# Optimization experiments

Hardware: AMD Instinct MI355X
Metric: run time of the kernel (lower is better)

The kernel has to match this reference:

```python
import jax, jax.numpy as jnp
import numpy as np

B, S, D, H = 32, 64, 256, 8
HD = D // H
NS = S + 1
TH = 0.5
LN_EPS = 1e-5


def _lin(k, out_d, in_d, gain=1.0):
    lim = gain * np.sqrt(6.0 / (in_d + out_d))
    return jax.random.uniform(k, (out_d, in_d), minval=-lim, maxval=lim, dtype=jnp.float32)


def setup_inputs() -> dict:
    key = jax.random.key(0)
    ks = jax.random.split(key, 16)
    g = 1.0 / np.sqrt(2.0)
    return {
        'desc_embeddings': jax.random.normal(ks[0], (B, S, D), dtype=jnp.float32),
        'name_value_embeddings': jax.random.normal(ks[1], (B, NS, D), dtype=jnp.float32),
        'Wg': _lin(ks[2], D, D), 'bg': jnp.zeros((D,), jnp.float32),
        'Wq': _lin(ks[3], D, D, g), 'bq': jnp.zeros((D,), jnp.float32),
        'Wk': _lin(ks[4], D, D, g), 'bk': jnp.zeros((D,), jnp.float32),
        'Wv': _lin(ks[5], D, D, g), 'bv': jnp.zeros((D,), jnp.float32),
        'We1': _lin(ks[6], D, 2 * D), 'be1': jnp.zeros((D,), jnp.float32),
        'lng': jnp.ones((D,), jnp.float32), 'lnb': jnp.zeros((D,), jnp.float32),
        'We2': _lin(ks[7], D, D), 'be2': jnp.zeros((D,), jnp.float32),
        'Wa': _lin(ks[8], 1, 3 * HD, g), 'ba': jnp.zeros((1,), jnp.float32),
        'Wo': _lin(ks[9], D, D, g), 'bo': jnp.zeros((D,), jnp.float32),
        'tb': jnp.zeros((1,), jnp.float32),
    }


def reference(desc_embeddings, name_value_embeddings, Wg, bg, Wq, bq, Wk, bk, Wv, bv,
              We1, be1, lng, lnb, We2, be2, Wa, ba, Wo, bo, tb):
    # 1. Global topology
    desc = desc_embeddings @ Wg.T + bg                      # [B,S,D]
    dn = desc / jnp.linalg.norm(desc, axis=-1, keepdims=True)
    gsim = jnp.einsum('bid,bjd->bij', dn, dn)
    gt = jax.nn.sigmoid(gsim + tb[0])
    # straight-through threshold
    A = (gt > TH).astype(gt.dtype) - jax.lax.stop_gradient(gt) + gt
    # 2. Sample-wise similarity
    var = name_value_embeddings[:, 1:, :]
    vn = var / jnp.linalg.norm(var, axis=-1, keepdims=True)
    ssim = jnp.einsum('bid,bjd->bij', vn, vn)
    A = A * (1.0 - jnp.eye(S, dtype=A.dtype))               # no self-interaction
    adjacency = jax.nn.softmax(A * ssim, axis=-1)
    # 4. Edge attrs & adjacency (scatter-assembled, CLS at index 0)
    var_edge = jnp.concatenate([
        jnp.broadcast_to(desc[:, :, None, :], (B, S, S, D)),
        jnp.broadcast_to(desc[:, None, :, :], (B, S, S, D))], axis=-1)  # [B,S,S,2D]
    cls_edge = jnp.concatenate([desc, desc], axis=-1)       # [B,S,2D]
    ea = jnp.zeros((B, NS, NS, 2 * D), jnp.float32)
    ea = ea.at[:, 1:, 1:].set(var_edge).at[:, 0, 1:].set(cls_edge).at[:, 1:, 0].set(cls_edge)
    na = jnp.zeros((B, NS, NS), jnp.float32)
    na = na.at[:, 1:, 1:].set(adjacency).at[:, 0, 1:].set(1.0)
    # 5. Attention
    q = (name_value_embeddings @ Wq.T + bq).reshape(B, NS, H, HD).transpose(0, 2, 1, 3)
    k = (name_value_embeddings @ Wk.T + bk).reshape(B, NS, H, HD).transpose(0, 2, 1, 3)
    v = (name_value_embeddings @ Wv.T + bv).reshape(B, NS, H, HD).transpose(0, 2, 1, 3)
    h = ea @ We1.T + be1
    mu = h.mean(axis=-1, keepdims=True)
    sig = ((h - mu) ** 2).mean(axis=-1, keepdims=True)
    h = (h - mu) / jnp.sqrt(sig + LN_EPS) * lng + lnb
    e = jax.nn.relu(h) @ We2.T + be2                        # [B,NS,NS,D]
    e = e.reshape(B, NS, NS, H, HD).transpose(0, 3, 1, 2, 4)  # [B,H,NS,NS,HD]
    e = e * na[:, None, :, :, None]
    # attn_proj(concat(q_i, k_j, e_ij)) decomposed into three dot products
    wq, wk_, we = Wa[0, :HD], Wa[0, HD:2 * HD], Wa[0, 2 * HD:]
    sq = jnp.einsum('bhid,d->bhi', q, wq)
    sk = jnp.einsum('bhjd,d->bhj', k, wk_)
    se = jnp.einsum('bhijd,d->bhij', e, we)
    scores = sq[:, :, :, None] + sk[:, :, None, :] + se + ba[0]
    scores = scores + (na[:, None, :, :] == 0).astype(scores.dtype) * -1e9
    aw = jax.nn.softmax(scores, axis=-1)                    # [B,H,NS,NS]
    ctx = jnp.einsum('bhij,bhjd->bhid', aw, v).transpose(0, 2, 1, 3).reshape(B, NS, D)
    out = ctx @ Wo.T + bo
    return (out, aw)
```

## Files before the change

### kernel.cpp

```cpp
#include <hip/hip_runtime.h>
#include <hip/hip_bf16.h>

#define BB 32
#define SS 64
#define DD 256
#define HH 8
#define HDIM 32
#define NSS 65
#define LN_EPS 1e-5f

#define OFF_DESC   0u
#define OFF_DESCT  524288u
#define OFF_U      1048576u
#define OFF_VT     1572864u
#define OFF_VART   2097152u
#define OFF_VBUF   2621440u
#define OFF_SQ     3153920u
#define OFF_SK     3170560u
#define OFF_CTX    3187200u
#define OFF_WGT    3719680u
#define OFF_WE1AT  3785216u
#define OFF_WE1BT  3850752u
#define OFF_WVT    3916288u
#define OFF_WOT    3981824u
#define OFF_CUT    4047360u
#define OFF_CVT    4112896u
#define OFF_BU     4178432u
#define OFF_BV     4178688u
#define OFF_WQF    4178944u
#define OFF_WKF    4180992u
#define OFF_CVEC   4183040u
#define OFF_RND    4183072u
#define OFF_RNV    4185120u
#define OFF_PKG    4187168u
#define OFF_PKM    4187680u

template <int R>
__device__ __forceinline__ void gemmR_body(const float* __restrict__ in,
                                           const float* __restrict__ WT,
                                           const float* __restrict__ bias,
                                           float* __restrict__ out,
                                           float* __restrict__ outT,
                                           int r0, int addBias, float* vals) {
    int o = threadIdx.x;
    const float* __restrict__ x = in + (size_t)r0 * DD;
    float acc[R];
    #pragma unroll
    for (int r = 0; r < R; ++r) acc[r] = 0.f;
    #pragma unroll 4
    for (int k = 0; k < DD; ++k) {
        float w = WT[(size_t)k * DD + o];
        #pragma unroll
        for (int r = 0; r < R; ++r)
            acc[r] = fmaf(x[r * DD + k], w, acc[r]);
    }
    float bb = addBias ? bias[o] : 0.f;
    #pragma unroll
    for (int r = 0; r < R; ++r) vals[r] = acc[r] + bb;
    if (out) {
        #pragma unroll
        for (int r = 0; r < R; ++r)
            out[(size_t)(r0 + r) * DD + o] = vals[r];
    }
    if (outT) {
        size_t base = (size_t)(r0 >> 6) * 16384 + (size_t)(o >> 2) * 256 + (o & 3);
        int j0 = r0 & 63;
        #pragma unroll
        for (int r = 0; r < R; ++r)
            outT[base + (size_t)(j0 + r) * 4] = vals[r];
    }
}

__global__ __launch_bounds__(256) void prep_a(
    const float* __restrict__ Wg, const float* __restrict__ We1,
    const float* __restrict__ Wv, const float* __restrict__ Wo,
    const float* __restrict__ Wq, const float* __restrict__ bq,
    const float* __restrict__ Wk, const float* __restrict__ bk,
    const float* __restrict__ We2, const float* __restrict__ be2,
    const float* __restrict__ Wa, const float* __restrict__ lng,
    const float* __restrict__ lnb,
    float* __restrict__ WgT, float* __restrict__ We1aT, float* __restrict__ We1bT,
    float* __restrict__ WvT, float* __restrict__ WoT,
    float* __restrict__ wqf, float* __restrict__ wkf,
    float* __restrict__ PKg, float* __restrict__ PKm, float* __restrict__ cvec) {
    __shared__ float t[64][65];
    int blk = blockIdx.x;
    if (blk < 80) {
        int which = blk >> 4, t16 = blk & 15;
        const float* src; float* dst; int ld, c0;
        if (which == 0)      { src = Wg;  dst = WgT;   ld = 256; c0 = 0; }
        else if (which == 1) { src = We1; dst = We1aT; ld = 512; c0 = 0; }
        else if (which == 2) { src = We1; dst = We1bT; ld = 512; c0 = 256; }
        else if (which == 3) { src = Wv;  dst = WvT;   ld = 256; c0 = 0; }
        else                 { src = Wo;  dst = WoT;   ld = 256; c0 = 0; }
        int to = t16 & 3, tk = t16 >> 2;
        int tx = threadIdx.x & 63, ty = threadIdx.x >> 6;
        #pragma unroll
        for (int r = ty; r < 64; r += 4)
            t[r][tx] = src[(size_t)(to * 64 + r) * ld + c0 + tk * 64 + tx];
        __syncthreads();
        #pragma unroll
        for (int r = ty; r < 64; r += 4)
            dst[(size_t)(tk * 64 + r) * DD + to * 64 + tx] = t[tx][r];
    } else if (blk < 88) {
        int h = blk - 80, in = threadIdx.x;
        float aq = 0.f, ak = 0.f, ae = 0.f;
        #pragma unroll
        for (int d = 0; d < HDIM; ++d) {
            aq = fmaf(Wq[(h * HDIM + d) * DD + in], Wa[d], aq);
            ak = fmaf(Wk[(h * HDIM + d) * DD + in], Wa[HDIM + d], ak);
            ae = fmaf(We2[(h * HDIM + d) * DD + in], Wa[2 * HDIM + d], ae);
        }
        wqf[h * DD + in] = aq;
        wkf[h * DD + in] = ak;
        PKm[in * HH + h] = ae;
        if (in == 0) {
            float cq = 0.f, ck = 0.f, ce = 0.f;
            for (int d = 0; d < HDIM; ++d) {
                cq = fmaf(bq[h * HDIM + d], Wa[d], cq);
                ck = fmaf(bk[h * HDIM + d], Wa[HDIM + d], ck);
                ce = fmaf(be2[h * HDIM + d], Wa[2 * HDIM + d], ce);
            }
            cvec[h] = cq; cvec[8 + h] = ck; cvec[16 + h] = ce;
        }
    } else {
        int d = threadIdx.x;
        PKg[d * 2] = lng[d];
        PKg[d * 2 + 1] = lnb[d];
    }
}

__global__ __launch_bounds__(256) void prep_b(
    const float* __restrict__ WgT, const float* __restrict__ We1aT,
    const float* __restrict__ We1bT, const float* __restrict__ bg,
    const float* __restrict__ be1,
    float* __restrict__ CuT, float* __restrict__ CvT,
    float* __restrict__ bu, float* __restrict__ bv) {
    float vals[16];
    int blk = blockIdx.x;
    if (blk < 16) gemmR_body<16>(WgT, We1aT, nullptr, CuT, nullptr, blk * 16, 0, vals);
    else if (blk < 32) gemmR_body<16>(WgT, We1bT, nullptr, CvT, nullptr, (blk - 16) * 16, 0, vals);
    else if (blk == 32) {
        int o = threadIdx.x;
        float a = be1[o];
        for (int m = 0; m < DD; ++m) a = fmaf(We1aT[(size_t)m * DD + o], bg[m], a);
        bu[o] = a;
    } else {
        int o = threadIdx.x;
        float a = 0.f;
        for (int m = 0; m < DD; ++m) a = fmaf(We1bT[(size_t)m * DD + o], bg[m], a);
        bv[o] = a;
    }
}

__global__ __launch_bounds__(256) void proj_kernel(
    const float* __restrict__ X, const float* __restrict__ nve,
    const float* __restrict__ WgT, const float* __restrict__ CuT,
    const float* __restrict__ CvT, const float* __restrict__ WvT,
    const float* __restrict__ bg, const float* __restrict__ bu,
    const float* __restrict__ bv, const float* __restrict__ bwv,
    const float* __restrict__ wqf, const float* __restrict__ wkf,
    const float* __restrict__ cvec,
    float* __restrict__ desc, float* __restrict__ descT,
    float* __restrict__ U, float* __restrict__ VT,
    float* __restrict__ varT, float* __restrict__ vbuf,
    float* __restrict__ sq, float* __restrict__ sk,
    float* __restrict__ rnd, float* __restrict__ rnv) {
    __shared__ float red[4][8];
    float vals[8];
    int blk = blockIdx.x;
    if (blk < 256) {
        gemmR_body<8>(X, WgT, bg, desc, descT, blk * 8, 1, vals);
        int w = threadIdx.x >> 6, lane = threadIdx.x & 63;
        #pragma unroll
        for (int r = 0; r < 8; ++r) {
            float s2 = vals[r] * vals[r];
            #pragma unroll
            for (int off = 32; off; off >>= 1) s2 += __shfl_xor(s2, off);
            if (lane == 0) red[w][r] = s2;
        }
        __syncthreads();
        if (threadIdx.x < 8) {
            float s = red[0][threadIdx.x] + red[1][threadIdx.x] +
                      red[2][threadIdx.x] + red[3][threadIdx.x];
            rnd[blk * 8 + threadIdx.x] = 1.f / sqrtf(s);
        }
    } else if (blk < 512) {
        gemmR_body<8>(X, CuT, bu, U, nullptr, (blk - 256) * 8, 1, vals);
    } else if (blk < 768) {
        gemmR_body<8>(X, CvT, bv, nullptr, VT, (blk - 512) * 8, 1, vals);
    } else if (blk < 1028) {
        gemmR_body<8>(nve, WvT, bwv, vbuf, nullptr, (blk - 768) * 8, 1, vals);
    } else if (blk < 1158) {
        int r0 = (blk - 1028) * 16;
        int lr = threadIdx.x >> 4, tq = threadIdx.x & 15;
        int g = r0 + lr, b = g / NSS, ii = g % NSS;
        const float* __restrict__ x = nve + (size_t)g * DD;
        const float* __restrict__ wv = ((tq < 8) ? wqf : wkf) + (tq & 7) * DD;
        float acc = 0.f;
        #pragma unroll 8
        for (int k = 0; k < DD; ++k) acc = fmaf(x[k], wv[k], acc);
        int h = tq & 7;
        if (tq < 8) sq[(size_t)(b * HH + h) * NSS + ii] = acc + cvec[h];
        else        sk[(size_t)(b * HH + h) * NSS + ii] = acc + cvec[8 + h];
    } else if (blk < 1286) {
        int r0 = (blk - 1158) * 16;
        int lr = threadIdx.x >> 4, tq = threadIdx.x & 15;
        int g = r0 + lr, b = g >> 6, s = g & 63;
        const float* __restrict__ x = nve + (size_t)(b * NSS + 1 + s) * DD;
        float ssum = 0.f;
        for (int k = tq; k < DD; k += 16) ssum = fmaf(x[k], x[k], ssum);
        ssum += __shfl_xor(ssum, 1);
        ssum += __shfl_xor(ssum, 2);
        ssum += __shfl_xor(ssum, 4);
        ssum += __shfl_xor(ssum, 8);
        if (tq == 0) rnv[g] = 1.f / sqrtf(ssum);
    } else {
        int b = blk - 1286;
        int d = threadIdx.x;
        size_t base = (size_t)b * 16384 + (size_t)(d >> 2) * 256 + (d & 3);
        const float* __restrict__ src = nve + ((size_t)b * NSS + 1) * DD + d;
        #pragma unroll 4
        for (int j = 0; j < 64; ++j)
            varT[base + (size_t)j * 4] = src[(size_t)j * DD];
    }
}

__global__ __launch_bounds__(256) void se_attn_kernel(
    const float* __restrict__ desc, const float* __restrict__ descT,
    const float* __restrict__ nve,  const float* __restrict__ varT,
    const float* __restrict__ U,    const float* __restrict__ VT,
    const float* __restrict__ vbuf,
    const float* __restrict__ rnd,  const float* __restrict__ rnv,
    const float* __restrict__ sq,   const float* __restrict__ sk,
    const float* __restrict__ PKg,  const float* __restrict__ PKm,
    const float* __restrict__ cvec, const float* __restrict__ ba,
    const float* __restrict__ tb,
    float* __restrict__ aw, float* __restrict__ ctx) {
    __shared__ float SH[4224];
    int t = blockIdx.x >> 5, b = blockIdx.x & 31;
    int w = threadIdx.x >> 6, lane = threadIdx.x & 63;
    float bav = ba[0];

    if (t < 16) {
        int iu = __builtin_amdgcn_readfirstlane(t * 4 + w);
        int i = iu + 1;
        const float4* __restrict__ dT4  = (const float4*)(descT + (size_t)b * 16384);
        const float4* __restrict__ vrT4 = (const float4*)(varT  + (size_t)b * 16384);
        const float4* __restrict__ vt4  = (const float4*)(VT    + (size_t)b * 16384);
        const float4* __restrict__ di4 = (const float4*)(desc + (size_t)(b * SS + iu) * DD);
        const float4* __restrict__ vi4 = (const float4*)(nve + (size_t)(b * NSS + 1 + iu) * DD);
        const float4* __restrict__ ui4 = (const float4*)(U + (size_t)(b * SS + iu) * DD);

        float gd = 0.f, vd = 0.f, ssum = 0.f, s2 = 0.f;
        #pragma unroll 4
        for (int f = 0; f < 64; ++f) {
            float4 a = dT4[f * 64 + lane];  float4 u1 = di4[f];
            float4 c = vrT4[f * 64 + lane]; float4 u2 = vi4[f];
            float4 v = vt4[f * 64 + lane];  float4 u = ui4[f];
            gd = fmaf(a.x, u1.x, gd); gd = fmaf(a.y, u1.y, gd);
            gd = fmaf(a.z, u1.z, gd); gd = fmaf(a.w, u1.w, gd);
            vd = fmaf(c.x, u2.x, vd); vd = fmaf(c.y, u2.y, vd);
            vd = fmaf(c.z, u2.z, vd); vd = fmaf(c.w, u2.w, vd);
            float t0 = v.x + u.x, t1 = v.y + u.y, t2 = v.z + u.z, t3 = v.w + u.w;
            ssum += (t0 + t1) + (t2 + t3);
            s2 = fmaf(t0, t0, s2); s2 = fmaf(t1, t1, s2);
            s2 = fmaf(t2, t2, s2); s2 = fmaf(t3, t3, s2);
        }
        float gsim = gd * rnd[b * SS + iu] * rnd[b * SS + lane];
        float ssim = vd * rnv[b * SS + iu] * rnv[b * SS + lane];
        bool flag = (gsim + tb[0] > 0.f) && (iu != lane);
        float P = flag ? ssim : 0.f;
        float e = __expf(P);
        float s = e;
        #pragma unroll
        for (int off = 32; off; off >>= 1) s += __shfl_xor(s, off);
        float nav = e / s;
        float mu = ssum * (1.f / DD);
        float var = fmaf(-mu, mu, s2 * (1.f / DD));
        float rstd = rsqrtf(var + LN_EPS);

        float p[HH];
        #pragma unroll
        for (int h = 0; h < HH; ++h) p[h] = 0.f;
        #pragma unroll 2
        for (int f = 0; f < 64; ++f) {
            float4 v = vt4[f * 64 + lane]; float4 u = ui4[f];
            const float4* __restrict__ pg = (const float4*)(PKg + 8 * f);
            float4 pg0 = pg[0], pg1 = pg[1];
            float tv[4] = {v.x + u.x, v.y + u.y, v.z + u.z, v.w + u.w};
            float gv[4] = {pg0.x, pg0.z, pg1.x, pg1.z};
            float bv_[4] = {pg0.y, pg0.w, pg1.y, pg1.w};
            #pragma unroll
            for (int c = 0; c < 4; ++c) {
                const float4* __restrict__ m4 = (const float4*)(PKm + (size_t)(4 * f + c) * HH);
                float4 mlo = m4[0], mhi = m4[1];
                float xn = fmaf((tv[c] - mu) * rstd, gv[c], bv_[c]);
                float r = fmaxf(xn, 0.f);
                p[0] = fmaf(r, mlo.x, p[0]); p[1] = fmaf(r, mlo.y, p[1]);
                p[2] = fmaf(r, mlo.z, p[2]); p[3] = fmaf(r, mlo.w, p[3]);
                p[4] = fmaf(r, mhi.x, p[4]); p[5] = fmaf(r, mhi.y, p[5]);
                p[6] = fmaf(r, mhi.z, p[6]); p[7] = fmaf(r, mhi.w, p[7]);
            }
        }

        float* awL = SH + w * 528;
        #pragma unroll
        for (int h = 0; h < HH; ++h) {
            float sev = nav * (p[h] + cvec[16 + h]);
            float sc = sq[(size_t)(b * HH + h) * NSS + i] +
                       sk[(size_t)(b * HH + h) * NSS + 1 + lane] + sev + bav;
            float m = sc;
            #pragma unroll
            for (int off = 32; off; off >>= 1) m = fmaxf(m, __shfl_xor(m, off));
            float e2 = __expf(sc - m);
            float tot = e2;
            #pragma unroll
            for (int off = 32; off; off >>= 1) tot += __shfl_xor(tot, off);
            float aval = e2 / tot;
            float* awrow = aw + ((size_t)(b * HH + h) * NSS + i) * NSS;
            awrow[1 + lane] = aval;
            if (lane == 0) awrow[0] = 0.f;
            awL[h * 66 + lane] = aval;
        }
        const float* __restrict__ awh = awL + (lane >> 3) * 66;
        const float4* __restrict__ vb4 = (const float4*)(vbuf + ((size_t)b * NSS + 1) * DD);
        float cx = 0.f, cy = 0.f, cz = 0.f, cw = 0.f;
        #pragma unroll 4
        for (int j = 0; j < 64; ++j) {
            float a = awh[j];
            float4 v = vb4[(size_t)j * 64 + lane];
            cx = fmaf(a, v.x, cx); cy = fmaf(a, v.y, cy);
            cz = fmaf(a, v.z, cz); cw = fmaf(a, v.w, cw);
        }
        *(float4*)(ctx + ((size_t)(b * NSS) + i) * DD + 4 * lane) =
            make_float4(cx, cy, cz, cw);
    } else {
        float* tile = SH;
        int dloc = lane & 31, jh = lane >> 5;
        float ss = 0.f, s2 = 0.f;
        for (int c = 0; c < 4; ++c) {
            for (int jr = w; jr < 64; jr += 4)
                tile[jr * 65 + lane] = U[(size_t)(b * SS + jr) * DD + c * 64 + lane];
            __syncthreads();
            #pragma unroll 8
            for (int dd = 0; dd < 64; ++dd) {
                int d = c * 64 + dd;
                float u = tile[lane * 65 + dd];
                float v = VT[(size_t)b * 16384 + (size_t)(d >> 2) * 256 + lane * 4 + (d & 3)];
                float t2 = u + v; ss += t2; s2 = fmaf(t2, t2, s2);
            }
            __syncthreads();
        }
        float mu = ss * (1.f / DD);
        float va = fmaf(-mu, mu, s2 * (1.f / DD));
        float rstd = rsqrtf(va + LN_EPS);
        float p[HH];
        #pragma unroll
        for (int h = 0; h < HH; ++h) p[h] = 0.f;
        for (int c = 0; c < 4; ++c) {
            for (int jr = w; jr < 64; jr += 4)
                tile[jr * 65 + lane] = U[(size_t)(b * SS + jr) * DD + c * 64 + lane];
            __syncthreads();
            #pragma unroll 4
            for (int dd = 0; dd < 64; ++dd) {
                int d = c * 64 + dd;
                float u = tile[lane * 65 + dd];
                float v = VT[(size_t)b * 16384 + (size_t)(d >> 2) * 256 + lane * 4 + (d & 3)];
                float t2 = u + v;
                float rv = fmaxf(fmaf((t2 - mu) * rstd, PKg[d * 2], PKg[d * 2 + 1]), 0.f);
                const float* __restrict__ m8 = PKm + (size_t)d * HH;
                #pragma unroll
                for (int h = 0; h < HH; ++h) p[h] = fmaf(rv, m8[h], p[h]);
            }
            __syncthreads();
        }
        float sel0 = 0.f, sel1 = 0.f;
        #pragma unroll
        for (int h = 0; h < HH; ++h) {
            if (h == w * 2)     sel0 = p[h];
            if (h == w * 2 + 1) sel1 = p[h];
        }
        #pragma unroll
        for (int q = 0; q < 2; ++q) {
            int h = w * 2 + q;
            float dot = q ? sel1 : sel0;
            float sev = dot + cvec[16 + h];
            float skh = sk[(size_t)(b * HH + h) * NSS + 1 + lane];
            float sc = sq[(size_t)(b * HH + h) * NSS] + skh + sev + bav;
            float m = sc;
            #pragma unroll
            for (int off = 32; off; off >>= 1) m = fmaxf(m, __shfl_xor(m, off));
            float e = __expf(sc - m), s = e;
            #pragma unroll
            for (int off = 32; off; off >>= 1) s += __shfl_xor(s, off);
            float aval = e / s;
            float* awrow = aw + ((size_t)(b * HH + h) * NSS) * NSS;
            awrow[1 + lane] = aval;
            if (lane == 0) awrow[0] = 0.f;
            float acc = 0.f;
            #pragma unroll
            for (int j2 = 0; j2 < 32; ++j2) {
                int jj = j2 * 2 + jh;
                float a = __shfl(aval, jj);
                acc = fmaf(a, vbuf[((size_t)(b * NSS) + 1 + jj) * DD + h * HDIM + dloc], acc);
            }
            acc += __shfl_xor(acc, 32);
            if (lane < 32)
                ctx[(size_t)(b * NSS) * DD + h * HDIM + dloc] = acc;
        }
    }
}

__global__ __launch_bounds__(256) void outgemm_kernel(
    const float* __restrict__ ctx, const float* __restrict__ WoT,
    const float* __restrict__ bo, float* __restrict__ out) {
    float vals[8];
    gemmR_body<8>(ctx, WoT, bo, out, nullptr, blockIdx.x * 8, 1, vals);
}

extern "C" void kernel_launch(void* const* d_in, const int* in_sizes, int n_in,
                              void* d_out, int out_size, void* d_ws, size_t ws_size,
                              hipStream_t stream) {
    const float* desc_emb = (const float*)d_in[0];
    const float* nve      = (const float*)d_in[1];
    const float* Wg  = (const float*)d_in[2];
    const float* bg  = (const float*)d_in[3];
    const float* Wq  = (const float*)d_in[4];
    const float* bq  = (const float*)d_in[5];
    const float* Wk  = (const float*)d_in[6];
    const float* bk  = (const float*)d_in[7];
    const float* Wv  = (const float*)d_in[8];
    const float* bv_in = (const float*)d_in[9];
    const float* We1 = (const float*)d_in[10];
    const float* be1 = (const float*)d_in[11];
    const float* lng = (const float*)d_in[12];
    const float* lnb = (const float*)d_in[13];
    const float* We2 = (const float*)d_in[14];
    const float* be2 = (const float*)d_in[15];
    const float* Wa  = (const float*)d_in[16];
    const float* ba  = (const float*)d_in[17];
    const float* Wo  = (const float*)d_in[18];
    const float* bo  = (const float*)d_in[19];
    const float* tb  = (const float*)d_in[20];

    float* ws    = (float*)d_ws;
    float* desc  = ws + OFF_DESC;
    float* descT = ws + OFF_DESCT;
    float* U     = ws + OFF_U;
    float* VT    = ws + OFF_VT;
    float* varT  = ws + OFF_VART;
    float* vbuf  = ws + OFF_VBUF;
    float* sq    = ws + OFF_SQ;
    float* sk    = ws + OFF_SK;
    float* ctx   = ws + OFF_CTX;
    float* WgT   = ws + OFF_WGT;
    float* We1aT = ws + OFF_WE1AT;
    float* We1bT = ws + OFF_WE1BT;
    float* WvT   = ws + OFF_WVT;
    float* WoT   = ws + OFF_WOT;
    float* CuT   = ws + OFF_CUT;
    float* CvT   = ws + OFF_CVT;
    float* bu    = ws + OFF_BU;
    float* bv    = ws + OFF_BV;
    float* wqf   = ws + OFF_WQF;
    float* wkf   = ws + OFF_WKF;
    float* cvec  = ws + OFF_CVEC;
    float* rnd   = ws + OFF_RND;
    float* rnv   = ws + OFF_RNV;
    float* PKg   = ws + OFF_PKG;
    float* PKm   = ws + OFF_PKM;

    float* out = (float*)d_out;
    float* aw  = out + (size_t)BB * NSS * DD;

    prep_a<<<89, 256, 0, stream>>>(Wg, We1, Wv, Wo, Wq, bq, Wk, bk, We2, be2,
                                   Wa, lng, lnb,
                                   WgT, We1aT, We1bT, WvT, WoT,
                                   wqf, wkf, PKg, PKm, cvec);
    prep_b<<<34, 256, 0, stream>>>(WgT, We1aT, We1bT, bg, be1, CuT, CvT, bu, bv);
    proj_kernel<<<1318, 256, 0, stream>>>(desc_emb, nve, WgT, CuT, CvT, WvT,
                                          bg, bu, bv, bv_in, wqf, wkf, cvec,
                                          desc, descT, U, VT, varT, vbuf,
                                          sq, sk, rnd, rnv);
    se_attn_kernel<<<544, 256, 0, stream>>>(desc, descT, nve, varT, U, VT,
                                            vbuf, rnd, rnv, sq, sk,
                                            PKg, PKm, cvec, ba, tb, aw, ctx);
    outgemm_kernel<<<260, 256, 0, stream>>>(ctx, WoT, bo, out);
}
```

Before: 146.2 us.

## Split adjacency/LayerNorm stats into separate kernel and halve heads per wave

Moves the per-row adjacency softmax and LayerNorm mean/rstd computation into a new adjln_kernel that writes them to scratch buffers that reuse dead weight-transpose workspace. The edge-score kernel then assigns each wave half of the heads (4 instead of 8), using a repacked interleaved gamma/beta/head-weight table, and splits the context reduction across two half-waves joined with a shuffle. This doubles the number of blocks to raise parallelism and cut per-thread register pressure. The cost is an extra launch, extra global round trips, and the LN/U+V reads being repeated for each head half.

```diff
diff --git a/kernel.cpp b/kernel.cpp
--- a/kernel.cpp
+++ b/kernel.cpp
@@ -34,6 +34,7 @@
 #define OFF_RNV    4185120u
 #define OFF_PKG    4187168u
 #define OFF_PKM    4187680u
+#define OFF_PKH    4189728u
 
 template <int R>
 __device__ __forceinline__ void gemmR_body(const float* __restrict__ in,
@@ -82,7 +83,8 @@
     float* __restrict__ WgT, float* __restrict__ We1aT, float* __restrict__ We1bT,
     float* __restrict__ WvT, float* __restrict__ WoT,
     float* __restrict__ wqf, float* __restrict__ wkf,
-    float* __restrict__ PKg, float* __restrict__ PKm, float* __restrict__ cvec) {
+    float* __restrict__ PKg, float* __restrict__ PKm, float* __restrict__ PKH,
+    float* __restrict__ cvec) {
     __shared__ float t[64][65];
     int blk = blockIdx.x;
     if (blk < 80) {
@@ -114,6 +116,7 @@
         wqf[h * DD + in] = aq;
         wkf[h * DD + in] = ak;
         PKm[in * HH + h] = ae;
+        PKH[((size_t)(h >> 2) * 256 + in) * 8 + 2 + (h & 3)] = ae;
         if (in == 0) {
             float cq = 0.f, ck = 0.f, ce = 0.f;
             for (int d = 0; d < HDIM; ++d) {
@@ -127,6 +130,14 @@
         int d = threadIdx.x;
         PKg[d * 2] = lng[d];
         PKg[d * 2 + 1] = lnb[d];
+        #pragma unroll
+        for (int hq = 0; hq < 2; ++hq) {
+            size_t base = ((size_t)hq * 256 + d) * 8;
+            PKH[base + 0] = lng[d];
+            PKH[base + 1] = lnb[d];
+            PKH[base + 6] = 0.f;
+            PKH[base + 7] = 0.f;
+        }
     }
 }
 
@@ -226,88 +237,106 @@
     }
 }
 
-__global__ __launch_bounds__(256) void se_attn_kernel(
+__global__ __launch_bounds__(256) void adjln_kernel(
     const float* __restrict__ desc, const float* __restrict__ descT,
     const float* __restrict__ nve,  const float* __restrict__ varT,
     const float* __restrict__ U,    const float* __restrict__ VT,
+    const float* __restrict__ rnd,  const float* __restrict__ rnv,
+    const float* __restrict__ tb,
+    float* __restrict__ navbuf, float* __restrict__ mubuf,
+    float* __restrict__ rstdbuf) {
+    int t = blockIdx.x >> 5, b = blockIdx.x & 31;
+    int w = threadIdx.x >> 6, lane = threadIdx.x & 63;
+    int iu = __builtin_amdgcn_readfirstlane(t * 4 + w);
+    const float4* __restrict__ dT4  = (const float4*)(descT + (size_t)b * 16384);
+    const float4* __restrict__ vrT4 = (const float4*)(varT  + (size_t)b * 16384);
+    const float4* __restrict__ vt4  = (const float4*)(VT    + (size_t)b * 16384);
+    const float4* __restrict__ di4 = (const float4*)(desc + (size_t)(b * SS + iu) * DD);
+    const float4* __restrict__ vi4 = (const float4*)(nve + (size_t)(b * NSS + 1 + iu) * DD);
+    const float4* __restrict__ ui4 = (const float4*)(U + (size_t)(b * SS + iu) * DD);
+    float gd = 0.f, vd = 0.f, ssum = 0.f, s2 = 0.f;
+    #pragma unroll 4
+    for (int f = 0; f < 64; ++f) {
+        float4 a = dT4[f * 64 + lane];  float4 u1 = di4[f];
+        float4 c = vrT4[f * 64 + lane]; float4 u2 = vi4[f];
+        float4 v = vt4[f * 64 + lane];  float4 u = ui4[f];
+        gd = fmaf(a.x, u1.x, gd); gd = fmaf(a.y, u1.y, gd);
+        gd = fmaf(a.z, u1.z, gd); gd = fmaf(a.w, u1.w, gd);
+        vd = fmaf(c.x, u2.x, vd); vd = fmaf(c.y, u2.y, vd);
+        vd = fmaf(c.z, u2.z, vd); vd = fmaf(c.w, u2.w, vd);
+        float t0 = v.x + u.x, t1 = v.y + u.y, t2 = v.z + u.z, t3 = v.w + u.w;
+        ssum += (t0 + t1) + (t2 + t3);
+        s2 = fmaf(t0, t0, s2); s2 = fmaf(t1, t1, s2);
+        s2 = fmaf(t2, t2, s2); s2 = fmaf(t3, t3, s2);
+    }
+    float gsim = gd * rnd[b * SS + iu] * rnd[b * SS + lane];
+    float ssim = vd * rnv[b * SS + iu] * rnv[b * SS + lane];
+    bool flag = (gsim + tb[0] > 0.f) && (iu != lane);
+    float P = flag ? ssim : 0.f;
+    float e = __expf(P);
+    float s = e;
+    #pragma unroll
+    for (int off = 32; off; off >>= 1) s += __shfl_xor(s, off);
+    float nav = e / s;
+    float mu = ssum * (1.f / DD);
+    float var = fmaf(-mu, mu, s2 * (1.f / DD));
+    float rstd = rsqrtf(var + LN_EPS);
+    size_t rowoff = (size_t)(b * SS + iu) * 64 + lane;
+    navbuf[rowoff] = nav;
+    mubuf[rowoff] = mu;
+    rstdbuf[rowoff] = rstd;
+}
+
+__global__ __launch_bounds__(256) void se_attn_kernel(
+    const float* __restrict__ U,    const float* __restrict__ VT,
     const float* __restrict__ vbuf,
-    const float* __restrict__ rnd,  const float* __restrict__ rnv,
     const float* __restrict__ sq,   const float* __restrict__ sk,
+    const float* __restrict__ PKH,
     const float* __restrict__ PKg,  const float* __restrict__ PKm,
     const float* __restrict__ cvec, const float* __restrict__ ba,
-    const float* __restrict__ tb,
+    const float* __restrict__ navbuf, const float* __restrict__ mubuf,
+    const float* __restrict__ rstdbuf,
     float* __restrict__ aw, float* __restrict__ ctx) {
     __shared__ float SH[4224];
-    int t = blockIdx.x >> 5, b = blockIdx.x & 31;
+    int bid = blockIdx.x;
     int w = threadIdx.x >> 6, lane = threadIdx.x & 63;
     float bav = ba[0];
 
-    if (t < 16) {
-        int iu = __builtin_amdgcn_readfirstlane(t * 4 + w);
+    if (bid < 1024) {
+        int t = bid >> 5, b = bid & 31;
+        int z = w >> 1, hq = w & 1;
+        int iu = __builtin_amdgcn_readfirstlane(t * 2 + z);
         int i = iu + 1;
-        const float4* __restrict__ dT4  = (const float4*)(descT + (size_t)b * 16384);
-        const float4* __restrict__ vrT4 = (const float4*)(varT  + (size_t)b * 16384);
-        const float4* __restrict__ vt4  = (const float4*)(VT    + (size_t)b * 16384);
-        const float4* __restrict__ di4 = (const float4*)(desc + (size_t)(b * SS + iu) * DD);
-        const float4* __restrict__ vi4 = (const float4*)(nve + (size_t)(b * NSS + 1 + iu) * DD);
+        size_t rowoff = (size_t)(b * SS + iu) * 64 + lane;
+        float nav = navbuf[rowoff];
+        float mu = mubuf[rowoff];
+        float rstd = rstdbuf[rowoff];
+        const float4* __restrict__ vt4 = (const float4*)(VT + (size_t)b * 16384);
         const float4* __restrict__ ui4 = (const float4*)(U + (size_t)(b * SS + iu) * DD);
-
-        float gd = 0.f, vd = 0.f, ssum = 0.f, s2 = 0.f;
-        #pragma unroll 4
-        for (int f = 0; f < 64; ++f) {
-            float4 a = dT4[f * 64 + lane];  float4 u1 = di4[f];
-            float4 c = vrT4[f * 64 + lane]; float4 u2 = vi4[f];
-            float4 v = vt4[f * 64 + lane];  float4 u = ui4[f];
-            gd = fmaf(a.x, u1.x, gd); gd = fmaf(a.y, u1.y, gd);
-            gd = fmaf(a.z, u1.z, gd); gd = fmaf(a.w, u1.w, gd);
-            vd = fmaf(c.x, u2.x, vd); vd = fmaf(c.y, u2.y, vd);
-            vd = fmaf(c.z, u2.z, vd); vd = fmaf(c.w, u2.w, vd);
-            float t0 = v.x + u.x, t1 = v.y + u.y, t2 = v.z + u.z, t3 = v.w + u.w;
-            ssum += (t0 + t1) + (t2 + t3);
-            s2 = fmaf(t0, t0, s2); s2 = fmaf(t1, t1, s2);
-            s2 = fmaf(t2, t2, s2); s2 = fmaf(t3, t3, s2);
-        }
-        float gsim = gd * rnd[b * SS + iu] * rnd[b * SS + lane];
-        float ssim = vd * rnv[b * SS + iu] * rnv[b * SS + lane];
-        bool flag = (gsim + tb[0] > 0.f) && (iu != lane);
-        float P = flag ? ssim : 0.f;
-        float e = __expf(P);
-        float s = e;
-        #pragma unroll
-        for (int off = 32; off; off >>= 1) s += __shfl_xor(s, off);
-        float nav = e / s;
-        float mu = ssum * (1.f / DD);
-        float var = fmaf(-mu, mu, s2 * (1.f / DD));
-        float rstd = rsqrtf(var + LN_EPS);
-
-        float p[HH];
-        #pragma unroll
-        for (int h = 0; h < HH; ++h) p[h] = 0.f;
+        const float4* __restrict__ ph = (const float4*)(PKH + (size_t)hq * 2048);
+
+        float p0 = 0.f, p1 = 0.f, p2 = 0.f, p3 = 0.f;
         #pragma unroll 2
         for (int f = 0; f < 64; ++f) {
             float4 v = vt4[f * 64 + lane]; float4 u = ui4[f];
-            const float4* __restrict__ pg = (const float4*)(PKg + 8 * f);
-            float4 pg0 = pg[0], pg1 = pg[1];
             float tv[4] = {v.x + u.x, v.y + u.y, v.z + u.z, v.w + u.w};
-            float gv[4] = {pg0.x, pg0.z, pg1.x, pg1.z};
-            float bv_[4] = {pg0.y, pg0.w, pg1.y, pg1.w};
             #pragma unroll
             for (int c = 0; c < 4; ++c) {
-                const float4* __restrict__ m4 = (const float4*)(PKm + (size_t)(4 * f + c) * HH);
-                float4 mlo = m4[0], mhi = m4[1];
-                float xn = fmaf((tv[c] - mu) * rstd, gv[c], bv_[c]);
+                float4 a = ph[(4 * f + c) * 2];
+                float4 b4 = ph[(4 * f + c) * 2 + 1];
+                float xn = fmaf((tv[c] - mu) * rstd, a.x, a.y);
                 float r = fmaxf(xn, 0.f);
-                p[0] = fmaf(r, mlo.x, p[0]); p[1] = fmaf(r, mlo.y, p[1]);
-                p[2] = fmaf(r, mlo.z, p[2]); p[3] = fmaf(r, mlo.w, p[3]);
-                p[4] = fmaf(r, mhi.x, p[4]); p[5] = fmaf(r, mhi.y, p[5]);
-                p[6] = fmaf(r, mhi.z, p[6]); p[7] = fmaf(r, mhi.w, p[7]);
+                p0 = fmaf(r, a.z, p0); p1 = fmaf(r, a.w, p1);
+                p2 = fmaf(r, b4.x, p2); p3 = fmaf(r, b4.y, p3);
             }
         }
-
-        float* awL = SH + w * 528;
-        #pragma unroll
-        for (int h = 0; h < HH; ++h) {
-            float sev = nav * (p[h] + cvec[16 + h]);
+        float psel[4] = {p0, p1, p2, p3};
+
+        float* awL = SH + w * 288;
+        #pragma unroll
+        for (int hh = 0; hh < 4; ++hh) {
+            int h = hq * 4 + hh;
+            float sev = nav * (psel[hh] + cvec[16 + h]);
             float sc = sq[(size_t)(b * HH + h) * NSS + i] +
                        sk[(size_t)(b * HH + h) * NSS + 1 + lane] + sev + bav;
             float m = sc;
@@ -321,21 +350,28 @@
             float* awrow = aw + ((size_t)(b * HH + h) * NSS + i) * NSS;
             awrow[1 + lane] = aval;
             if (lane == 0) awrow[0] = 0.f;
-            awL[h * 66 + lane] = aval;
-        }
-        const float* __restrict__ awh = awL + (lane >> 3) * 66;
+            awL[hh * 66 + lane] = aval;
+        }
+
+        int q32 = lane & 31, jh = lane >> 5;
+        const float* __restrict__ awh = awL + (q32 >> 3) * 66;
         const float4* __restrict__ vb4 = (const float4*)(vbuf + ((size_t)b * NSS + 1) * DD);
         float cx = 0.f, cy = 0.f, cz = 0.f, cw = 0.f;
-        #pragma unroll 4
-        for (int j = 0; j < 64; ++j) {
-            float a = awh[j];
-            float4 v = vb4[(size_t)j * 64 + lane];
-            cx = fmaf(a, v.x, cx); cy = fmaf(a, v.y, cy);
-            cz = fmaf(a, v.z, cz); cw = fmaf(a, v.w, cw);
-        }
-        *(float4*)(ctx + ((size_t)(b * NSS) + i) * DD + 4 * lane) =
-            make_float4(cx, cy, cz, cw);
+        #pragma unroll 8
+        for (int j2 = 0; j2 < 32; ++j2) {
+            int j = j2 * 2 + jh;
+            float a2 = awh[j];
+            float4 v = vb4[(size_t)j * 64 + hq * 32 + q32];
+            cx = fmaf(a2, v.x, cx); cy = fmaf(a2, v.y, cy);
+            cz = fmaf(a2, v.z, cz); cw = fmaf(a2, v.w, cw);
+        }
+        cx += __shfl_xor(cx, 32); cy += __shfl_xor(cy, 32);
+        cz += __shfl_xor(cz, 32); cw += __shfl_xor(cw, 32);
+        if (lane < 32)
+            *(float4*)(ctx + ((size_t)(b * NSS) + i) * DD + (hq * 32 + q32) * 4) =
+                make_float4(cx, cy, cz, cw);
     } else {
+        int b = bid - 1024;
         float* tile = SH;
         int dloc = lane & 31, jh = lane >> 5;
         float ss = 0.f, s2 = 0.f;
@@ -470,6 +506,13 @@
     float* rnv   = ws + OFF_RNV;
     float* PKg   = ws + OFF_PKG;
     float* PKm   = ws + OFF_PKM;
+    float* PKH   = ws + OFF_PKH;
+    float* navbuf  = ws + OFF_WGT;
+    float* mubuf   = ws + OFF_WE1AT;
+    float* rstdbuf = ws + OFF_CUT;
+    navbuf  = ws + OFF_WGT;
+    mubuf   = ws + OFF_WE1BT;
+    rstdbuf = ws + OFF_CUT;
 
     float* out = (float*)d_out;
     float* aw  = out + (size_t)BB * NSS * DD;
@@ -477,14 +520,16 @@
     prep_a<<<89, 256, 0, stream>>>(Wg, We1, Wv, Wo, Wq, bq, Wk, bk, We2, be2,
                                    Wa, lng, lnb,
                                    WgT, We1aT, We1bT, WvT, WoT,
-                                   wqf, wkf, PKg, PKm, cvec);
+                                   wqf, wkf, PKg, PKm, PKH, cvec);
     prep_b<<<34, 256, 0, stream>>>(WgT, We1aT, We1bT, bg, be1, CuT, CvT, bu, bv);
     proj_kernel<<<1318, 256, 0, stream>>>(desc_emb, nve, WgT, CuT, CvT, WvT,
                                           bg, bu, bv, bv_in, wqf, wkf, cvec,
                                           desc, descT, U, VT, varT, vbuf,
                                           sq, sk, rnd, rnv);
-    se_attn_kernel<<<544, 256, 0, stream>>>(desc, descT, nve, varT, U, VT,
-                                            vbuf, rnd, rnv, sq, sk,
-                                            PKg, PKm, cvec, ba, tb, aw, ctx);
+    adjln_kernel<<<512, 256, 0, stream>>>(desc, descT, nve, varT, U, VT,
+                                          rnd, rnv, tb, navbuf, mubuf, rstdbuf);
+    se_attn_kernel<<<1056, 256, 0, stream>>>(U, VT, vbuf, sq, sk, PKH, PKg, PKm,
+                                             cvec, ba, navbuf, mubuf, rstdbuf,
+                                             aw, ctx);
     outgemm_kernel<<<260, 256, 0, stream>>>(ctx, WoT, bo, out);
 }
```

Result: slower. 235.5 us (+61.1%).

## Split pairwise stats into separate kernel with two-row register blocking

Applied to the files above, without the earlier changes.

Moves the gsim/ssim dot products and the LayerNorm mean/variance computation out of se_attn_kernel into a new stats_kernel. Each wave there handles two query rows, so every transposed column load is reused twice. LayerNorm moments are expanded algebraically into per-row sums of U (computed in proj_kernel), per-column sums of V, and the cross term U·V. This avoids recomputing (v+u) squares but adds a kernel launch and global round-trips for the nav/mu/rstd buffers. Those buffers reuse workspace regions that previously held weights (WgT, We1bT, CuT), which are no longer read after proj_kernel.

```diff
diff --git a/kernel.cpp b/kernel.cpp
--- a/kernel.cpp
+++ b/kernel.cpp
@@ -34,6 +34,8 @@
 #define OFF_RNV    4185120u
 #define OFF_PKG    4187168u
 #define OFF_PKM    4187680u
+#define OFF_SU     4189728u
+#define OFF_SUU    4191776u
 
 template <int R>
 __device__ __forceinline__ void gemmR_body(const float* __restrict__ in,
@@ -165,8 +167,10 @@
     float* __restrict__ U, float* __restrict__ VT,
     float* __restrict__ varT, float* __restrict__ vbuf,
     float* __restrict__ sq, float* __restrict__ sk,
-    float* __restrict__ rnd, float* __restrict__ rnv) {
+    float* __restrict__ rnd, float* __restrict__ rnv,
+    float* __restrict__ SU, float* __restrict__ SUU) {
     __shared__ float red[4][8];
+    __shared__ float red2[4][8];
     float vals[8];
     int blk = blockIdx.x;
     if (blk < 256) {
@@ -187,6 +191,26 @@
         }
     } else if (blk < 512) {
         gemmR_body<8>(X, CuT, bu, U, nullptr, (blk - 256) * 8, 1, vals);
+        int w = threadIdx.x >> 6, lane = threadIdx.x & 63;
+        #pragma unroll
+        for (int r = 0; r < 8; ++r) {
+            float s1 = vals[r];
+            float s2 = vals[r] * vals[r];
+            #pragma unroll
+            for (int off = 32; off; off >>= 1) {
+                s1 += __shfl_xor(s1, off);
+                s2 += __shfl_xor(s2, off);
+            }
+            if (lane == 0) { red[w][r] = s1; red2[w][r] = s2; }
+        }
+        __syncthreads();
+        if (threadIdx.x < 8) {
+            int r0 = (blk - 256) * 8;
+            SU[r0 + threadIdx.x] = red[0][threadIdx.x] + red[1][threadIdx.x] +
+                                   red[2][threadIdx.x] + red[3][threadIdx.x];
+            SUU[r0 + threadIdx.x] = red2[0][threadIdx.x] + red2[1][threadIdx.x] +
+                                    red2[2][threadIdx.x] + red2[3][threadIdx.x];
+        }
     } else if (blk < 768) {
         gemmR_body<8>(X, CvT, bv, nullptr, VT, (blk - 512) * 8, 1, vals);
     } else if (blk < 1028) {
@@ -226,16 +250,89 @@
     }
 }
 
-__global__ __launch_bounds__(256) void se_attn_kernel(
+__global__ __launch_bounds__(256) void stats_kernel(
     const float* __restrict__ desc, const float* __restrict__ descT,
     const float* __restrict__ nve,  const float* __restrict__ varT,
     const float* __restrict__ U,    const float* __restrict__ VT,
+    const float* __restrict__ rnd,  const float* __restrict__ rnv,
+    const float* __restrict__ SU,   const float* __restrict__ SUU,
+    const float* __restrict__ tb,
+    float* __restrict__ navbuf, float* __restrict__ mubuf,
+    float* __restrict__ rstdbuf) {
+    int t = blockIdx.x >> 5, b = blockIdx.x & 31;
+    int w = threadIdx.x >> 6, lane = threadIdx.x & 63;
+    int i0 = __builtin_amdgcn_readfirstlane(t * 8 + w * 2);
+    const float4* __restrict__ dT4  = (const float4*)(descT + (size_t)b * 16384);
+    const float4* __restrict__ vrT4 = (const float4*)(varT  + (size_t)b * 16384);
+    const float4* __restrict__ vt4  = (const float4*)(VT    + (size_t)b * 16384);
+    const float4* __restrict__ x0 = (const float4*)(desc + (size_t)(b * SS + i0) * DD);
+    const float4* __restrict__ x1 = x0 + 64;
+    const float4* __restrict__ y0 = (const float4*)(nve + (size_t)(b * NSS + 1 + i0) * DD);
+    const float4* __restrict__ y1 = y0 + 64;
+    const float4* __restrict__ z0 = (const float4*)(U + (size_t)(b * SS + i0) * DD);
+    const float4* __restrict__ z1 = z0 + 64;
+    float g10 = 0.f, g11 = 0.f, g20 = 0.f, g21 = 0.f, g30 = 0.f, g31 = 0.f;
+    float sv = 0.f, svv = 0.f;
+    #pragma unroll 4
+    for (int f = 0; f < 64; ++f) {
+        float4 a = dT4[f * 64 + lane];
+        float4 p0 = x0[f], p1 = x1[f];
+        g10 = fmaf(a.x, p0.x, g10); g10 = fmaf(a.y, p0.y, g10);
+        g10 = fmaf(a.z, p0.z, g10); g10 = fmaf(a.w, p0.w, g10);
+        g11 = fmaf(a.x, p1.x, g11); g11 = fmaf(a.y, p1.y, g11);
+        g11 = fmaf(a.z, p1.z, g11); g11 = fmaf(a.w, p1.w, g11);
+        float4 c = vrT4[f * 64 + lane];
+        float4 q0 = y0[f], q1 = y1[f];
+        g20 = fmaf(c.x, q0.x, g20); g20 = fmaf(c.y, q0.y, g20);
+        g20 = fmaf(c.z, q0.z, g20); g20 = fmaf(c.w, q0.w, g20);
+        g21 = fmaf(c.x, q1.x, g21); g21 = fmaf(c.y, q1.y, g21);
+        g21 = fmaf(c.z, q1.z, g21); g21 = fmaf(c.w, q1.w, g21);
+        float4 v = vt4[f * 64 + lane];
+        float4 r0 = z0[f], r1 = z1[f];
+        g30 = fmaf(v.x, r0.x, g30); g30 = fmaf(v.y, r0.y, g30);
+        g30 = fmaf(v.z, r0.z, g30); g30 = fmaf(v.w, r0.w, g30);
+        g31 = fmaf(v.x, r1.x, g31); g31 = fmaf(v.y, r1.y, g31);
+        g31 = fmaf(v.z, r1.z, g31); g31 = fmaf(v.w, r1.w, g31);
+        sv += (v.x + v.y) + (v.z + v.w);
+        svv = fmaf(v.x, v.x, svv); svv = fmaf(v.y, v.y, svv);
+        svv = fmaf(v.z, v.z, svv); svv = fmaf(v.w, v.w, svv);
+    }
+    float tbv = tb[0];
+    float rj = rnd[b * SS + lane], rvj = rnv[b * SS + lane];
+    #pragma unroll
+    for (int r = 0; r < 2; ++r) {
+        int ir = i0 + r;
+        float g1 = r ? g11 : g10;
+        float g2 = r ? g21 : g20;
+        float g3 = r ? g31 : g30;
+        float gsim = g1 * rnd[b * SS + ir] * rj;
+        float ssim = g2 * rnv[b * SS + ir] * rvj;
+        bool flag = (gsim + tbv > 0.f) && (ir != lane);
+        float P = flag ? ssim : 0.f;
+        float e = __expf(P);
+        float s = e;
+        #pragma unroll
+        for (int off = 32; off; off >>= 1) s += __shfl_xor(s, off);
+        float nav = e / s;
+        float mu = (sv + SU[b * SS + ir]) * (1.f / DD);
+        float var = fmaf(-mu, mu,
+                         (svv + 2.f * g3 + SUU[b * SS + ir]) * (1.f / DD));
+        float rstd = rsqrtf(var + LN_EPS);
+        size_t rowoff = (size_t)(b * SS + ir) * 64 + lane;
+        navbuf[rowoff] = nav;
+        mubuf[rowoff] = mu;
+        rstdbuf[rowoff] = rstd;
+    }
+}
+
+__global__ __launch_bounds__(256) void se_attn_kernel(
+    const float* __restrict__ U,    const float* __restrict__ VT,
     const float* __restrict__ vbuf,
-    const float* __restrict__ rnd,  const float* __restrict__ rnv,
     const float* __restrict__ sq,   const float* __restrict__ sk,
     const float* __restrict__ PKg,  const float* __restrict__ PKm,
     const float* __restrict__ cvec, const float* __restrict__ ba,
-    const float* __restrict__ tb,
+    const float* __restrict__ navbuf, const float* __restrict__ mubuf,
+    const float* __restrict__ rstdbuf,
     float* __restrict__ aw, float* __restrict__ ctx) {
     __shared__ float SH[4224];
     int t = blockIdx.x >> 5, b = blockIdx.x & 31;
@@ -245,40 +342,12 @@
     if (t < 16) {
         int iu = __builtin_amdgcn_readfirstlane(t * 4 + w);
         int i = iu + 1;
-        const float4* __restrict__ dT4  = (const float4*)(descT + (size_t)b * 16384);
-        const float4* __restrict__ vrT4 = (const float4*)(varT  + (size_t)b * 16384);
-        const float4* __restrict__ vt4  = (const float4*)(VT    + (size_t)b * 16384);
-        const float4* __restrict__ di4 = (const float4*)(desc + (size_t)(b * SS + iu) * DD);
-        const float4* __restrict__ vi4 = (const float4*)(nve + (size_t)(b * NSS + 1 + iu) * DD);
+        size_t rowoff = (size_t)(b * SS + iu) * 64 + lane;
+        float nav = navbuf[rowoff];
+        float mu = mubuf[rowoff];
+        float rstd = rstdbuf[rowoff];
+        const float4* __restrict__ vt4 = (const float4*)(VT + (size_t)b * 16384);
         const float4* __restrict__ ui4 = (const float4*)(U + (size_t)(b * SS + iu) * DD);
-
-        float gd = 0.f, vd = 0.f, ssum = 0.f, s2 = 0.f;
-        #pragma unroll 4
-        for (int f = 0; f < 64; ++f) {
-            float4 a = dT4[f * 64 + lane];  float4 u1 = di4[f];
-            float4 c = vrT4[f * 64 + lane]; float4 u2 = vi4[f];
-            float4 v = vt4[f * 64 + lane];  float4 u = ui4[f];
-            gd = fmaf(a.x, u1.x, gd); gd = fmaf(a.y, u1.y, gd);
-            gd = fmaf(a.z, u1.z, gd); gd = fmaf(a.w, u1.w, gd);
-            vd = fmaf(c.x, u2.x, vd); vd = fmaf(c.y, u2.y, vd);
-            vd = fmaf(c.z, u2.z, vd); vd = fmaf(c.w, u2.w, vd);
-            float t0 = v.x + u.x, t1 = v.y + u.y, t2 = v.z + u.z, t3 = v.w + u.w;
-            ssum += (t0 + t1) + (t2 + t3);
-            s2 = fmaf(t0, t0, s2); s2 = fmaf(t1, t1, s2);
-            s2 = fmaf(t2, t2, s2); s2 = fmaf(t3, t3, s2);
-        }
-        float gsim = gd * rnd[b * SS + iu] * rnd[b * SS + lane];
-        float ssim = vd * rnv[b * SS + iu] * rnv[b * SS + lane];
-        bool flag = (gsim + tb[0] > 0.f) && (iu != lane);
-        float P = flag ? ssim : 0.f;
-        float e = __expf(P);
-        float s = e;
-        #pragma unroll
-        for (int off = 32; off; off >>= 1) s += __shfl_xor(s, off);
-        float nav = e / s;
-        float mu = ssum * (1.f / DD);
-        float var = fmaf(-mu, mu, s2 * (1.f / DD));
-        float rstd = rsqrtf(var + LN_EPS);
 
         float p[HH];
         #pragma unroll
@@ -470,6 +539,11 @@
     float* rnv   = ws + OFF_RNV;
     float* PKg   = ws + OFF_PKG;
     float* PKm   = ws + OFF_PKM;
+    float* SU    = ws + OFF_SU;
+    float* SUU   = ws + OFF_SUU;
+    float* navbuf  = ws + OFF_WGT;
+    float* mubuf   = ws + OFF_WE1BT;
+    float* rstdbuf = ws + OFF_CUT;
 
     float* out = (float*)d_out;
     float* aw  = out + (size_t)BB * NSS * DD;
@@ -482,9 +556,12 @@
     proj_kernel<<<1318, 256, 0, stream>>>(desc_emb, nve, WgT, CuT, CvT, WvT,
                                           bg, bu, bv, bv_in, wqf, wkf, cvec,
                                           desc, descT, U, VT, varT, vbuf,
-                                          sq, sk, rnd, rnv);
-    se_attn_kernel<<<544, 256, 0, stream>>>(desc, descT, nve, varT, U, VT,
-                                            vbuf, rnd, rnv, sq, sk,
-                                            PKg, PKm, cvec, ba, tb, aw, ctx);
+                                          sq, sk, rnd, rnv, SU, SUU);
+    stats_kernel<<<256, 256, 0, stream>>>(desc, descT, nve, varT, U, VT,
+                                          rnd, rnv, SU, SUU, tb,
+                                          navbuf, mubuf, rstdbuf);
+    se_attn_kernel<<<544, 256, 0, stream>>>(U, VT, vbuf, sq, sk, PKg, PKm,
+                                            cvec, ba, navbuf, mubuf, rstdbuf,
+                                            aw, ctx);
     outgemm_kernel<<<260, 256, 0, stream>>>(ctx, WoT, bo, out);
 }
```

Result: slower. 162.5 us (+11.1%).

## Move input-only side jobs into the prep kernels and unroll the GEMM loop more

Applied to the files above, without the earlier changes.

The rnv norm and varT transpose blocks depend only on inputs, so they move into prep_a. The sq/sk projection blocks, which need only prep_a outputs, move into prep_b. This fills the small, underused prep launches and shrinks proj_kernel to its four GEMM sections. The gemmR inner loop unroll also rises from 4 to 8, which may raise register pressure.

```diff
diff --git a/kernel.cpp b/kernel.cpp
--- a/kernel.cpp
+++ b/kernel.cpp
@@ -47,7 +47,7 @@
     float acc[R];
     #pragma unroll
     for (int r = 0; r < R; ++r) acc[r] = 0.f;
-    #pragma unroll 4
+    #pragma unroll 8
     for (int k = 0; k < DD; ++k) {
         float w = WT[(size_t)k * DD + o];
         #pragma unroll
@@ -78,11 +78,12 @@
     const float* __restrict__ Wk, const float* __restrict__ bk,
     const float* __restrict__ We2, const float* __restrict__ be2,
     const float* __restrict__ Wa, const float* __restrict__ lng,
-    const float* __restrict__ lnb,
+    const float* __restrict__ lnb, const float* __restrict__ nve,
     float* __restrict__ WgT, float* __restrict__ We1aT, float* __restrict__ We1bT,
     float* __restrict__ WvT, float* __restrict__ WoT,
     float* __restrict__ wqf, float* __restrict__ wkf,
-    float* __restrict__ PKg, float* __restrict__ PKm, float* __restrict__ cvec) {
+    float* __restrict__ PKg, float* __restrict__ PKm, float* __restrict__ cvec,
+    float* __restrict__ rnv, float* __restrict__ varT) {
     __shared__ float t[64][65];
     int blk = blockIdx.x;
     if (blk < 80) {
@@ -123,88 +124,12 @@
             }
             cvec[h] = cq; cvec[8 + h] = ck; cvec[16 + h] = ce;
         }
-    } else {
+    } else if (blk == 88) {
         int d = threadIdx.x;
         PKg[d * 2] = lng[d];
         PKg[d * 2 + 1] = lnb[d];
-    }
-}
-
-__global__ __launch_bounds__(256) void prep_b(
-    const float* __restrict__ WgT, const float* __restrict__ We1aT,
-    const float* __restrict__ We1bT, const float* __restrict__ bg,
-    const float* __restrict__ be1,
-    float* __restrict__ CuT, float* __restrict__ CvT,
-    float* __restrict__ bu, float* __restrict__ bv) {
-    float vals[16];
-    int blk = blockIdx.x;
-    if (blk < 16) gemmR_body<16>(WgT, We1aT, nullptr, CuT, nullptr, blk * 16, 0, vals);
-    else if (blk < 32) gemmR_body<16>(WgT, We1bT, nullptr, CvT, nullptr, (blk - 16) * 16, 0, vals);
-    else if (blk == 32) {
-        int o = threadIdx.x;
-        float a = be1[o];
-        for (int m = 0; m < DD; ++m) a = fmaf(We1aT[(size_t)m * DD + o], bg[m], a);
-        bu[o] = a;
-    } else {
-        int o = threadIdx.x;
-        float a = 0.f;
-        for (int m = 0; m < DD; ++m) a = fmaf(We1bT[(size_t)m * DD + o], bg[m], a);
-        bv[o] = a;
-    }
-}
-
-__global__ __launch_bounds__(256) void proj_kernel(
-    const float* __restrict__ X, const float* __restrict__ nve,
-    const float* __restrict__ WgT, const float* __restrict__ CuT,
-    const float* __restrict__ CvT, const float* __restrict__ WvT,
-    const float* __restrict__ bg, const float* __restrict__ bu,
-    const float* __restrict__ bv, const float* __restrict__ bwv,
-    const float* __restrict__ wqf, const float* __restrict__ wkf,
-    const float* __restrict__ cvec,
-    float* __restrict__ desc, float* __restrict__ descT,
-    float* __restrict__ U, float* __restrict__ VT,
-    float* __restrict__ varT, float* __restrict__ vbuf,
-    float* __restrict__ sq, float* __restrict__ sk,
-    float* __restrict__ rnd, float* __restrict__ rnv) {
-    __shared__ float red[4][8];
-    float vals[8];
-    int blk = blockIdx.x;
-    if (blk < 256) {
-        gemmR_body<8>(X, WgT, bg, desc, descT, blk * 8, 1, vals);
-        int w = threadIdx.x >> 6, lane = threadIdx.x & 63;
-        #pragma unroll
-        for (int r = 0; r < 8; ++r) {
-            float s2 = vals[r] * vals[r];
-            #pragma unroll
-            for (int off = 32; off; off >>= 1) s2 += __shfl_xor(s2, off);
-            if (lane == 0) red[w][r] = s2;
-        }
-        __syncthreads();
-        if (threadIdx.x < 8) {
-            float s = red[0][threadIdx.x] + red[1][threadIdx.x] +
-                      red[2][threadIdx.x] + red[3][threadIdx.x];
-            rnd[blk * 8 + threadIdx.x] = 1.f / sqrtf(s);
-        }
-    } else if (blk < 512) {
-        gemmR_body<8>(X, CuT, bu, U, nullptr, (blk - 256) * 8, 1, vals);
-    } else if (blk < 768) {
-        gemmR_body<8>(X, CvT, bv, nullptr, VT, (blk - 512) * 8, 1, vals);
-    } else if (blk < 1028) {
-        gemmR_body<8>(nve, WvT, bwv, vbuf, nullptr, (blk - 768) * 8, 1, vals);
-    } else if (blk < 1158) {
-        int r0 = (blk - 1028) * 16;
-        int lr = threadIdx.x >> 4, tq = threadIdx.x & 15;
-        int g = r0 + lr, b = g / NSS, ii = g % NSS;
-        const float* __restrict__ x = nve + (size_t)g * DD;
-        const float* __restrict__ wv = ((tq < 8) ? wqf : wkf) + (tq & 7) * DD;
-        float acc = 0.f;
-        #pragma unroll 8
-        for (int k = 0; k < DD; ++k) acc = fmaf(x[k], wv[k], acc);
-        int h = tq & 7;
-        if (tq < 8) sq[(size_t)(b * HH + h) * NSS + ii] = acc + cvec[h];
-        else        sk[(size_t)(b * HH + h) * NSS + ii] = acc + cvec[8 + h];
-    } else if (blk < 1286) {
-        int r0 = (blk - 1158) * 16;
+    } else if (blk < 217) {
+        int r0 = (blk - 89) * 16;
         int lr = threadIdx.x >> 4, tq = threadIdx.x & 15;
         int g = r0 + lr, b = g >> 6, s = g & 63;
         const float* __restrict__ x = nve + (size_t)(b * NSS + 1 + s) * DD;
@@ -216,13 +141,88 @@
         ssum += __shfl_xor(ssum, 8);
         if (tq == 0) rnv[g] = 1.f / sqrtf(ssum);
     } else {
-        int b = blk - 1286;
+        int b = blk - 217;
         int d = threadIdx.x;
         size_t base = (size_t)b * 16384 + (size_t)(d >> 2) * 256 + (d & 3);
         const float* __restrict__ src = nve + ((size_t)b * NSS + 1) * DD + d;
         #pragma unroll 4
         for (int j = 0; j < 64; ++j)
             varT[base + (size_t)j * 4] = src[(size_t)j * DD];
+    }
+}
+
+__global__ __launch_bounds__(256) void prep_b(
+    const float* __restrict__ WgT, const float* __restrict__ We1aT,
+    const float* __restrict__ We1bT, const float* __restrict__ bg,
+    const float* __restrict__ be1, const float* __restrict__ nve,
+    const float* __restrict__ wqf, const float* __restrict__ wkf,
+    const float* __restrict__ cvec,
+    float* __restrict__ CuT, float* __restrict__ CvT,
+    float* __restrict__ bu, float* __restrict__ bv,
+    float* __restrict__ sq, float* __restrict__ sk) {
+    float vals[16];
+    int blk = blockIdx.x;
+    if (blk < 16) gemmR_body<16>(WgT, We1aT, nullptr, CuT, nullptr, blk * 16, 0, vals);
+    else if (blk < 32) gemmR_body<16>(WgT, We1bT, nullptr, CvT, nullptr, (blk - 16) * 16, 0, vals);
+    else if (blk == 32) {
+        int o = threadIdx.x;
+        float a = be1[o];
+        for (int m = 0; m < DD; ++m) a = fmaf(We1aT[(size_t)m * DD + o], bg[m], a);
+        bu[o] = a;
+    } else if (blk == 33) {
+        int o = threadIdx.x;
+        float a = 0.f;
+        for (int m = 0; m < DD; ++m) a = fmaf(We1bT[(size_t)m * DD + o], bg[m], a);
+        bv[o] = a;
+    } else {
+        int r0 = (blk - 34) * 16;
+        int lr = threadIdx.x >> 4, tq = threadIdx.x & 15;
+        int g = r0 + lr, b = g / NSS, ii = g % NSS;
+        const float* __restrict__ x = nve + (size_t)g * DD;
+        const float* __restrict__ wv = ((tq < 8) ? wqf : wkf) + (tq & 7) * DD;
+        float acc = 0.f;
+        #pragma unroll 8
+        for (int k = 0; k < DD; ++k) acc = fmaf(x[k], wv[k], acc);
+        int h = tq & 7;
+        if (tq < 8) sq[(size_t)(b * HH + h) * NSS + ii] = acc + cvec[h];
+        else        sk[(size_t)(b * HH + h) * NSS + ii] = acc + cvec[8 + h];
+    }
+}
+
+__global__ __launch_bounds__(256) void proj_kernel(
+    const float* __restrict__ X, const float* __restrict__ nve,
+    const float* __restrict__ WgT, const float* __restrict__ CuT,
+    const float* __restrict__ CvT, const float* __restrict__ WvT,
+    const float* __restrict__ bg, const float* __restrict__ bu,
+    const float* __restrict__ bv, const float* __restrict__ bwv,
+    float* __restrict__ desc, float* __restrict__ descT,
+    float* __restrict__ U, float* __restrict__ VT,
+    float* __restrict__ vbuf, float* __restrict__ rnd) {
+    __shared__ float red[4][8];
+    float vals[8];
+    int blk = blockIdx.x;
+    if (blk < 256) {
+        gemmR_body<8>(X, WgT, bg, desc, descT, blk * 8, 1, vals);
+        int w = threadIdx.x >> 6, lane = threadIdx.x & 63;
+        #pragma unroll
+        for (int r = 0; r < 8; ++r) {
+            float s2 = vals[r] * vals[r];
+            #pragma unroll
+            for (int off = 32; off; off >>= 1) s2 += __shfl_xor(s2, off);
+            if (lane == 0) red[w][r] = s2;
+        }
+        __syncthreads();
+        if (threadIdx.x < 8) {
+            float s = red[0][threadIdx.x] + red[1][threadIdx.x] +
+                      red[2][threadIdx.x] + red[3][threadIdx.x];
+            rnd[blk * 8 + threadIdx.x] = 1.f / sqrtf(s);
+        }
+    } else if (blk < 512) {
+        gemmR_body<8>(X, CuT, bu, U, nullptr, (blk - 256) * 8, 1, vals);
+    } else if (blk < 768) {
+        gemmR_body<8>(X, CvT, bv, nullptr, VT, (blk - 512) * 8, 1, vals);
+    } else {
+        gemmR_body<8>(nve, WvT, bwv, vbuf, nullptr, (blk - 768) * 8, 1, vals);
     }
 }
 
@@ -474,15 +474,16 @@
     float* out = (float*)d_out;
     float* aw  = out + (size_t)BB * NSS * DD;
 
-    prep_a<<<89, 256, 0, stream>>>(Wg, We1, Wv, Wo, Wq, bq, Wk, bk, We2, be2,
-                                   Wa, lng, lnb,
-                                   WgT, We1aT, We1bT, WvT, WoT,
-                                   wqf, wkf, PKg, PKm, cvec);
-    prep_b<<<34, 256, 0, stream>>>(WgT, We1aT, We1bT, bg, be1, CuT, CvT, bu, bv);
-    proj_kernel<<<1318, 256, 0, stream>>>(desc_emb, nve, WgT, CuT, CvT, WvT,
-                                          bg, bu, bv, bv_in, wqf, wkf, cvec,
-                                          desc, descT, U, VT, varT, vbuf,
-                                          sq, sk, rnd, rnv);
+    prep_a<<<249, 256, 0, stream>>>(Wg, We1, Wv, Wo, Wq, bq, Wk, bk, We2, be2,
+                                    Wa, lng, lnb, nve,
+                                    WgT, We1aT, We1bT, WvT, WoT,
+                                    wqf, wkf, PKg, PKm, cvec, rnv, varT);
+    prep_b<<<164, 256, 0, stream>>>(WgT, We1aT, We1bT, bg, be1, nve,
+                                    wqf, wkf, cvec,
+                                    CuT, CvT, bu, bv, sq, sk);
+    proj_kernel<<<1028, 256, 0, stream>>>(desc_emb, nve, WgT, CuT, CvT, WvT,
+                                          bg, bu, bv, bv_in,
+                                          desc, descT, U, VT, vbuf, rnd);
     se_attn_kernel<<<544, 256, 0, stream>>>(desc, descT, nve, varT, U, VT,
                                             vbuf, rnd, rnv, sq, sk,
                                             PKg, PKm, cvec, ba, tb, aw, ctx);
```

After: 151.4 us. 1.04x slower.
